# Performance work log

Hardware: AMD Instinct MI355X
Metric: run time of the kernel (lower is better)

Reference implementation:

```python
import jax, jax.numpy as jnp
import numpy as np

N = 4096
D = 512   # d_model == dff (required by the original code path)
H = 4
NEG = -1e10
ALPHA = 0.3  # keras LeakyReLU default alpha


def setup_inputs() -> dict:
    key = jax.random.key(0)
    ks = jax.random.split(key, 8)
    nodes = jax.random.normal(ks[0], (N, D), dtype=jnp.float32)
    # sparse-ish 0/1 dense adjacency with self loops
    adj = (jax.random.uniform(ks[1], (N, N)) < 0.01).astype(jnp.float32)
    adj = jnp.maximum(adj, jnp.eye(N, dtype=jnp.float32))
    s = 0.05
    W_node = jax.random.normal(ks[2], (D, D), dtype=jnp.float32) * s
    b_node = jnp.zeros((D,), dtype=jnp.float32)
    K = jax.random.normal(ks[3], (H, D, D), dtype=jnp.float32) * s
    A_self = jax.random.normal(ks[4], (H, D), dtype=jnp.float32) * s
    A_neigh = jax.random.normal(ks[5], (H, D), dtype=jnp.float32) * s
    return {"nodes": nodes, "adj": adj, "W_node": W_node, "b_node": b_node,
            "K": K, "A_self": A_self, "A_neigh": A_neigh, "num_heads": H}


def reference(nodes, adj, W_node, b_node, K, A_self, A_neigh, num_heads):
    # node_layer: Dense(dff)
    x = nodes @ W_node + b_node                       # [N, D]
    # per-head projection, vectorized over heads
    feats = jnp.einsum('nd,hdf->hnf', x, K)           # [H, N, D]
    # additive attention scores; both terms are per-row scalars -> [H, N]
    s = jnp.einsum('hnf,hf->hn', feats, A_self) + jnp.einsum('hnf,hf->hn', feats, A_neigh)
    s = jnp.where(s > 0, s, ALPHA * s)                # LeakyReLU(alpha=0.3)
    # broadcast row score over columns + adjacency mask, softmax over neighbors
    logits = s[:, :, None] + NEG * (1.0 - adj)[None]  # [H, N, N]
    attn = jax.nn.softmax(logits, axis=-1)
    # dropout is identity at inference (training=False)
    out = jnp.einsum('hij,hjf->hif', attn, feats)     # [H, N, D]
    out = jnp.mean(out, axis=0)                       # mean over heads
    return jax.nn.relu(out)
```

## Files before the change

kernel.cpp:

```cpp
#include <hip/hip_runtime.h>


typedef short  short8 __attribute__((ext_vector_type(8)));
typedef float  f32x4  __attribute__((ext_vector_type(4)));

__device__ inline unsigned short f2bf(float f) {
    union { float f; unsigned int u; } v; v.f = f;
    unsigned int u = v.u;
    u += 0x7fffu + ((u >> 16) & 1u);
    return (unsigned short)(u >> 16);
}

__device__ inline void gl_lds16(const void* gp, void* lp) {
    __builtin_amdgcn_global_load_lds(
        (const __attribute__((address_space(1))) void*)gp,
        (__attribute__((address_space(3))) void*)lp, 16, 0, 0);
}

__global__ __launch_bounds__(256) void prep_kernel(
        const float* __restrict__ nodes, const float* __restrict__ adj,
        const float* __restrict__ W, const float* __restrict__ b,
        const float* __restrict__ K,
        unsigned short* __restrict__ MmatT, float* __restrict__ bias2,
        unsigned short* __restrict__ nodesBf,
        int* __restrict__ degArr, int* __restrict__ nbrArr,
        int N, int D, int H, int numCast) {
    __shared__ unsigned short As[64][40];
    __shared__ unsigned short Bs[64][40];
    __shared__ float red[4][64];
    __shared__ int lst[1024];
    __shared__ int cnt;

    const int bid = blockIdx.x;
    const int tid = threadIdx.x;
    const int DD  = D * D;
    const int lane = tid & 63, wave = tid >> 6;
    const int wy = wave >> 1, wx = wave & 1;
    const int l15 = lane & 15, quad = lane >> 4;

    if (bid < 64) {
        const int by = bid >> 3, bx = bid & 7;
        const int f0 = by * 64, d0 = bx * 64;
        const float invH = 1.0f / (float)H;
        const int kk = tid >> 3;
        const int ff = (tid & 7) * 8;
        const int dr = tid >> 2;
        const int dk = (tid & 3) * 8;

        float4 kc[4][2], wc[2];
#pragma unroll
        for (int h = 0; h < 4; ++h) {
            const float* kp = K + ((size_t)h * D + kk) * D + f0 + ff;
            kc[h][0] = *reinterpret_cast<const float4*>(kp);
            kc[h][1] = *reinterpret_cast<const float4*>(kp + 4);
        }
        {
            const float* wp = W + (size_t)(d0 + dr) * D + dk;
            wc[0] = *reinterpret_cast<const float4*>(wp);
            wc[1] = *reinterpret_cast<const float4*>(wp + 4);
        }

        f32x4 acc[2][2] = {};
#pragma unroll
        for (int k0 = 0; k0 < 512; k0 += 32) {
            float4 kn[4][2], wn[2];
            if (k0 + 32 < 512) {
#pragma unroll
                for (int h = 0; h < 4; ++h) {
                    const float* kp = K + ((size_t)h * D + (k0 + 32 + kk)) * D + f0 + ff;
                    kn[h][0] = *reinterpret_cast<const float4*>(kp);
                    kn[h][1] = *reinterpret_cast<const float4*>(kp + 4);
                }
                const float* wp = W + (size_t)(d0 + dr) * D + (k0 + 32) + dk;
                wn[0] = *reinterpret_cast<const float4*>(wp);
                wn[1] = *reinterpret_cast<const float4*>(wp + 4);
            }
            float s[8];
#pragma unroll
            for (int j = 0; j < 4; ++j) {
                s[j]     = kc[0][0][j] + kc[1][0][j] + kc[2][0][j] + kc[3][0][j];
                s[j + 4] = kc[0][1][j] + kc[1][1][j] + kc[2][1][j] + kc[3][1][j];
            }
            short8 bv;
#pragma unroll
            for (int j = 0; j < 4; ++j) {
                bv[j]     = (short)f2bf(wc[0][j]);
                bv[j + 4] = (short)f2bf(wc[1][j]);
            }
            __syncthreads();
#pragma unroll
            for (int j = 0; j < 8; ++j)
                As[ff + j][kk] = f2bf(s[j] * invH);
            *reinterpret_cast<short8*>(&Bs[dr][dk]) = bv;
            __syncthreads();
            short8 a0 = *reinterpret_cast<const short8*>(&As[wy * 32 +      l15][quad * 8]);
            short8 a1 = *reinterpret_cast<const short8*>(&As[wy * 32 + 16 + l15][quad * 8]);
            short8 b0 = *reinterpret_cast<const short8*>(&Bs[wx * 32 +      l15][quad * 8]);
            short8 b1 = *reinterpret_cast<const short8*>(&Bs[wx * 32 + 16 + l15][quad * 8]);
            acc[0][0] = __builtin_amdgcn_mfma_f32_16x16x32_bf16(a0, b0, acc[0][0], 0, 0, 0);
            acc[0][1] = __builtin_amdgcn_mfma_f32_16x16x32_bf16(a0, b1, acc[0][1], 0, 0, 0);
            acc[1][0] = __builtin_amdgcn_mfma_f32_16x16x32_bf16(a1, b0, acc[1][0], 0, 0, 0);
            acc[1][1] = __builtin_amdgcn_mfma_f32_16x16x32_bf16(a1, b1, acc[1][1], 0, 0, 0);
            if (k0 + 32 < 512) {
#pragma unroll
                for (int h = 0; h < 4; ++h) { kc[h][0] = kn[h][0]; kc[h][1] = kn[h][1]; }
                wc[0] = wn[0]; wc[1] = wn[1];
            }
        }
#pragma unroll
        for (int mi = 0; mi < 2; ++mi)
#pragma unroll
            for (int ni = 0; ni < 2; ++ni) {
                int col = d0 + wx * 32 + ni * 16 + l15;
#pragma unroll
                for (int r = 0; r < 4; ++r) {
                    int row = f0 + wy * 32 + mi * 16 + quad * 4 + r;
                    MmatT[(size_t)row * D + col] = f2bf(acc[mi][ni][r]);
                }
            }
    } else if (bid < 72) {
        const int f0 = (bid - 64) * 64;
        const int fl = tid & 63, grp = tid >> 6;
        const float invH = 1.0f / (float)H;
        float a = 0.f;
        for (int d = grp; d < D; d += 4) {
            const float* kp = K + (size_t)d * D + f0 + fl;
            float v = 0.f;
#pragma unroll
            for (int h = 0; h < 4; ++h) v += kp[(size_t)h * DD];
            a += b[d] * v;
        }
        red[grp][fl] = a;
        __syncthreads();
        if (tid < 64)
            bias2[f0 + tid] = (red[0][tid] + red[1][tid] + red[2][tid] + red[3][tid]) * invH;
    } else if (bid < 72 + N) {
        const int row = bid - 72;
        if (tid == 0) cnt = 0;
        __syncthreads();
        const float4* ap = reinterpret_cast<const float4*>(adj + (size_t)row * N);
        float4 av[4];
#pragma unroll
        for (int c = 0; c < 4; ++c) av[c] = ap[c * 256 + tid];
#pragma unroll
        for (int c = 0; c < 4; ++c) {
            int b4 = (c * 256 + tid) * 4;
            if (av[c].x > 0.5f) { int p = atomicAdd(&cnt, 1); if (p < 1024) lst[p] = b4;     }
            if (av[c].y > 0.5f) { int p = atomicAdd(&cnt, 1); if (p < 1024) lst[p] = b4 + 1; }
            if (av[c].z > 0.5f) { int p = atomicAdd(&cnt, 1); if (p < 1024) lst[p] = b4 + 2; }
            if (av[c].w > 0.5f) { int p = atomicAdd(&cnt, 1); if (p < 1024) lst[p] = b4 + 3; }
        }
        __syncthreads();
        int deg = cnt; if (deg > 1024) deg = 1024;
        if (tid == 0) degArr[row] = deg;
        for (int i = tid; i < deg; i += 256)
            nbrArr[(size_t)row * 1024 + i] = lst[i];
    } else {
        const int total  = (N * D) >> 3;
        const int stride = numCast << 8;
        for (int i = (bid - 72 - N) * 256 + tid; i < total; i += stride) {
            const float* p = nodes + (size_t)i * 8;
            float4 x = *reinterpret_cast<const float4*>(p);
            float4 y = *reinterpret_cast<const float4*>(p + 4);
            short8 o;
            o[0] = (short)f2bf(x.x); o[1] = (short)f2bf(x.y);
            o[2] = (short)f2bf(x.z); o[3] = (short)f2bf(x.w);
            o[4] = (short)f2bf(y.x); o[5] = (short)f2bf(y.y);
            o[6] = (short)f2bf(y.z); o[7] = (short)f2bf(y.w);
            *reinterpret_cast<short8*>(nodesBf + (size_t)i * 8) = o;
        }
    }
}

__global__ __launch_bounds__(256) void gemm2_kernel(
        const unsigned short* __restrict__ nodesBf,
        const unsigned short* __restrict__ MmatT,
        const float* __restrict__ bias2, unsigned short* __restrict__ g, int D) {
    __shared__ unsigned short As[2][64][32];
    __shared__ unsigned short Bs[2][64][32];
    const int bid = blockIdx.x;
    const int lb = (bid & 7) * 64 + (bid >> 3);
    const int by = lb >> 3, bx = lb & 7;
    const int tid = threadIdx.x;
    const int lane = tid & 63, wave = tid >> 6;
    const int wy = wave >> 1, wx = wave & 1;
    const int l15 = lane & 15, quad = lane >> 4;

    const int cgl = ((tid & 3) ^ ((tid >> 3) & 3)) * 8;
    const unsigned short* Ag = nodesBf + (size_t)(by * 64 + (tid >> 2)) * D + cgl;
    const unsigned short* Bg = MmatT   + (size_t)(bx * 64 + (tid >> 2)) * D + cgl;
    unsigned short* AsW0 = &As[0][0][0] + wave * 512;
    unsigned short* AsW1 = &As[1][0][0] + wave * 512;
    unsigned short* BsW0 = &Bs[0][0][0] + wave * 512;
    unsigned short* BsW1 = &Bs[1][0][0] + wave * 512;

    f32x4 acc[2][2] = {};
    gl_lds16(Ag, AsW0);
    gl_lds16(Bg, BsW0);

    const int ra = wy * 32 + l15, rb = wx * 32 + l15;
    const int qa = (quad ^ ((ra >> 1) & 3)) * 8;
    const int qb = (quad ^ ((rb >> 1) & 3)) * 8;

    int cur = 0;
#pragma unroll
    for (int k0 = 0; k0 < 512; k0 += 32) {
        if (k0 + 32 < 512) {
            gl_lds16(Ag + k0 + 32, cur ? AsW0 : AsW1);
            gl_lds16(Bg + k0 + 32, cur ? BsW0 : BsW1);
            asm volatile("s_waitcnt vmcnt(2)" ::: "memory");
        } else {
            asm volatile("s_waitcnt vmcnt(0)" ::: "memory");
        }
        __builtin_amdgcn_s_barrier();
        __builtin_amdgcn_sched_barrier(0);
        const unsigned short* Af = cur ? &As[1][0][0] : &As[0][0][0];
        const unsigned short* Bf = cur ? &Bs[1][0][0] : &Bs[0][0][0];
        short8 a0 = *reinterpret_cast<const short8*>(Af + (ra     ) * 32 + qa);
        short8 a1 = *reinterpret_cast<const short8*>(Af + (ra + 16) * 32 + qa);
        short8 b0 = *reinterpret_cast<const short8*>(Bf + (rb     ) * 32 + qb);
        short8 b1 = *reinterpret_cast<const short8*>(Bf + (rb + 16) * 32 + qb);
        acc[0][0] = __builtin_amdgcn_mfma_f32_16x16x32_bf16(a0, b0, acc[0][0], 0, 0, 0);
        acc[0][1] = __builtin_amdgcn_mfma_f32_16x16x32_bf16(a0, b1, acc[0][1], 0, 0, 0);
        acc[1][0] = __builtin_amdgcn_mfma_f32_16x16x32_bf16(a1, b0, acc[1][0], 0, 0, 0);
        acc[1][1] = __builtin_amdgcn_mfma_f32_16x16x32_bf16(a1, b1, acc[1][1], 0, 0, 0);
        __builtin_amdgcn_sched_barrier(0);
        asm volatile("s_waitcnt lgkmcnt(0)" ::: "memory");
        __builtin_amdgcn_s_barrier();
        cur ^= 1;
    }

#pragma unroll
    for (int mi = 0; mi < 2; ++mi)
#pragma unroll
        for (int ni = 0; ni < 2; ++ni) {
            int col = bx * 64 + wx * 32 + ni * 16 + l15;
            float bvl = bias2[col];
#pragma unroll
            for (int r = 0; r < 4; ++r) {
                int row = by * 64 + wy * 32 + mi * 16 + quad * 4 + r;
                g[(size_t)row * D + col] = f2bf(acc[mi][ni][r] + bvl);
            }
        }
}

__global__ __launch_bounds__(256) void aggregate_kernel(
        const int* __restrict__ degArr, const int* __restrict__ nbrArr,
        const unsigned short* __restrict__ g, float* __restrict__ out,
        int N, int D) {
    const int row = blockIdx.x;
    const int tid = threadIdx.x;
    __shared__ int lst[1024];
    const int deg = degArr[row];
    for (int i = tid; i < deg; i += 256) lst[i] = nbrArr[(size_t)row * 1024 + i];
    __syncthreads();

    const int col = tid * 2;
    float acc0 = 0.f, acc1 = 0.f;
    int k = 0;
    for (; k + 8 <= deg; k += 8) {
        unsigned int u[8];
#pragma unroll
        for (int j = 0; j < 8; ++j)
            u[j] = *reinterpret_cast<const unsigned int*>(&g[(size_t)lst[k + j] * D + col]);
#pragma unroll
        for (int j = 0; j < 8; ++j) {
            union { unsigned int i; float f; } lo, hi;
            lo.i = u[j] << 16; hi.i = u[j] & 0xffff0000u;
            acc0 += lo.f; acc1 += hi.f;
        }
    }
    for (; k < deg; ++k) {
        unsigned int u = *reinterpret_cast<const unsigned int*>(&g[(size_t)lst[k] * D + col]);
        union { unsigned int i; float f; } lo, hi;
        lo.i = u << 16; hi.i = u & 0xffff0000u;
        acc0 += lo.f; acc1 += hi.f;
    }

    float inv = deg > 0 ? 1.f / (float)deg : 0.f;
    acc0 *= inv; acc1 *= inv;
    float2 o;
    o.x = acc0 > 0.f ? acc0 : 0.f;
    o.y = acc1 > 0.f ? acc1 : 0.f;
    *reinterpret_cast<float2*>(&out[(size_t)row * D + col]) = o;
}

extern "C" void kernel_launch(void* const* d_in, const int* in_sizes, int n_in,
                              void* d_out, int out_size, void* d_ws, size_t ws_size,
                              hipStream_t stream) {
    const float* nodes  = (const float*)d_in[0];
    const float* adj    = (const float*)d_in[1];
    const float* W_node = (const float*)d_in[2];
    const float* b_node = (const float*)d_in[3];
    const float* K      = (const float*)d_in[4];

    const int D  = in_sizes[3];
    const int N  = in_sizes[0] / D;
    const int H  = in_sizes[4] / (D * D);
    const int DD = D * D;

    float* out = (float*)d_out;

    char* ws = (char*)d_ws;
    unsigned short* MmatT   = (unsigned short*)(ws);
    size_t off = (size_t)DD * 2;
    float*          bias2   = (float*)(ws + off);          off += (size_t)D * 4;
    unsigned short* nodesBf = (unsigned short*)(ws + off); off += (size_t)N * D * 2;
    unsigned short* g_bf16  = (unsigned short*)(ws + off); off += (size_t)N * D * 2;
    int*            degArr  = (int*)(ws + off);            off += (size_t)N * 4;
    int*            nbrArr  = (int*)(ws + off);

    const int numCast = 952;
    prep_kernel<<<dim3(64 + 8 + N + numCast), 256, 0, stream>>>(
        nodes, adj, W_node, b_node, K, MmatT, bias2, nodesBf, degArr, nbrArr,
        N, D, H, numCast);

    gemm2_kernel<<<dim3((N / 64) * (D / 64)), 256, 0, stream>>>(
        nodesBf, MmatT, bias2, g_bf16, D);

    aggregate_kernel<<<dim3(N), 256, 0, stream>>>(degArr, nbrArr, g_bf16, out, N, D);
}
```

Measured before the change: 158.6 us.

## Double prep kernel block size and split weight-fold GEMM K across two halves

Launches the prep kernel with 512 threads per block. In the weight-fold GEMM, the two 256-thread halves each handle half of the K dimension, and the partial tiles are combined through shared memory. The adjacency scan and cast blocks now read 8 floats per thread, and the bias reduction uses 8 groups. The cast grid shrinks to 512 blocks. The GEMM loses its register prefetch and adds a reduction step, and the shared-memory union changes occupancy.

```diff
diff --git a/kernel.cpp b/kernel.cpp
--- a/kernel.cpp
+++ b/kernel.cpp
@@ -17,7 +17,7 @@
         (__attribute__((address_space(3))) void*)lp, 16, 0, 0);
 }
 
-__global__ __launch_bounds__(256) void prep_kernel(
+__global__ __launch_bounds__(512, 4) void prep_kernel(
         const float* __restrict__ nodes, const float* __restrict__ adj,
         const float* __restrict__ W, const float* __restrict__ b,
         const float* __restrict__ K,
@@ -25,148 +25,163 @@
         unsigned short* __restrict__ nodesBf,
         int* __restrict__ degArr, int* __restrict__ nbrArr,
         int N, int D, int H, int numCast) {
-    __shared__ unsigned short As[64][40];
-    __shared__ unsigned short Bs[64][40];
-    __shared__ float red[4][64];
-    __shared__ int lst[1024];
+    __shared__ union {
+        struct {
+            unsigned short As[2][64][40];
+            unsigned short Bs[2][64][40];
+        } g;
+        float red64[64][64];
+        int   lst[1024];
+    } sm;
+    __shared__ float red2[8][64];
     __shared__ int cnt;
 
     const int bid = blockIdx.x;
     const int tid = threadIdx.x;
     const int DD  = D * D;
     const int lane = tid & 63, wave = tid >> 6;
-    const int wy = wave >> 1, wx = wave & 1;
     const int l15 = lane & 15, quad = lane >> 4;
 
     if (bid < 64) {
         const int by = bid >> 3, bx = bid & 7;
         const int f0 = by * 64, d0 = bx * 64;
         const float invH = 1.0f / (float)H;
-        const int kk = tid >> 3;
-        const int ff = (tid & 7) * 8;
-        const int dr = tid >> 2;
-        const int dk = (tid & 3) * 8;
-
-        float4 kc[4][2], wc[2];
-#pragma unroll
-        for (int h = 0; h < 4; ++h) {
-            const float* kp = K + ((size_t)h * D + kk) * D + f0 + ff;
-            kc[h][0] = *reinterpret_cast<const float4*>(kp);
-            kc[h][1] = *reinterpret_cast<const float4*>(kp + 4);
-        }
-        {
-            const float* wp = W + (size_t)(d0 + dr) * D + dk;
-            wc[0] = *reinterpret_cast<const float4*>(wp);
-            wc[1] = *reinterpret_cast<const float4*>(wp + 4);
-        }
+        const int h  = tid >> 8;
+        const int th = tid & 255;
+        const int wy = (wave >> 1) & 1, wx = wave & 1;
+        const int kk = th >> 3;
+        const int ff = (th & 7) * 8;
+        const int dr = th >> 2;
+        const int dk = (th & 3) * 8;
+        const int kh = h * 256;
 
         f32x4 acc[2][2] = {};
-#pragma unroll
-        for (int k0 = 0; k0 < 512; k0 += 32) {
-            float4 kn[4][2], wn[2];
-            if (k0 + 32 < 512) {
-#pragma unroll
-                for (int h = 0; h < 4; ++h) {
-                    const float* kp = K + ((size_t)h * D + (k0 + 32 + kk)) * D + f0 + ff;
-                    kn[h][0] = *reinterpret_cast<const float4*>(kp);
-                    kn[h][1] = *reinterpret_cast<const float4*>(kp + 4);
-                }
-                const float* wp = W + (size_t)(d0 + dr) * D + (k0 + 32) + dk;
-                wn[0] = *reinterpret_cast<const float4*>(wp);
-                wn[1] = *reinterpret_cast<const float4*>(wp + 4);
-            }
+        for (int k0 = 0; k0 < 256; k0 += 32) {
+            f32x4 kv[4][2];
+#pragma unroll
+            for (int hh = 0; hh < 4; ++hh) {
+                const float* kp = K + ((size_t)hh * D + (kh + k0 + kk)) * D + f0 + ff;
+                kv[hh][0] = *reinterpret_cast<const f32x4*>(kp);
+                kv[hh][1] = *reinterpret_cast<const f32x4*>(kp + 4);
+            }
+            const float* wp = W + (size_t)(d0 + dr) * D + kh + k0 + dk;
+            f32x4 wu = *reinterpret_cast<const f32x4*>(wp);
+            f32x4 wv = *reinterpret_cast<const f32x4*>(wp + 4);
+
             float s[8];
 #pragma unroll
             for (int j = 0; j < 4; ++j) {
-                s[j]     = kc[0][0][j] + kc[1][0][j] + kc[2][0][j] + kc[3][0][j];
-                s[j + 4] = kc[0][1][j] + kc[1][1][j] + kc[2][1][j] + kc[3][1][j];
+                s[j]     = kv[0][0][j] + kv[1][0][j] + kv[2][0][j] + kv[3][0][j];
+                s[j + 4] = kv[0][1][j] + kv[1][1][j] + kv[2][1][j] + kv[3][1][j];
             }
             short8 bv;
 #pragma unroll
             for (int j = 0; j < 4; ++j) {
-                bv[j]     = (short)f2bf(wc[0][j]);
-                bv[j + 4] = (short)f2bf(wc[1][j]);
+                bv[j]     = (short)f2bf(wu[j]);
+                bv[j + 4] = (short)f2bf(wv[j]);
             }
             __syncthreads();
 #pragma unroll
             for (int j = 0; j < 8; ++j)
-                As[ff + j][kk] = f2bf(s[j] * invH);
-            *reinterpret_cast<short8*>(&Bs[dr][dk]) = bv;
+                sm.g.As[h][ff + j][kk] = f2bf(s[j] * invH);
+            *reinterpret_cast<short8*>(&sm.g.Bs[h][dr][dk]) = bv;
             __syncthreads();
-            short8 a0 = *reinterpret_cast<const short8*>(&As[wy * 32 +      l15][quad * 8]);
-            short8 a1 = *reinterpret_cast<const short8*>(&As[wy * 32 + 16 + l15][quad * 8]);
-            short8 b0 = *reinterpret_cast<const short8*>(&Bs[wx * 32 +      l15][quad * 8]);
-            short8 b1 = *reinterpret_cast<const short8*>(&Bs[wx * 32 + 16 + l15][quad * 8]);
+            short8 a0 = *reinterpret_cast<const short8*>(&sm.g.As[h][wy * 32 +      l15][quad * 8]);
+            short8 a1 = *reinterpret_cast<const short8*>(&sm.g.As[h][wy * 32 + 16 + l15][quad * 8]);
+            short8 b0 = *reinterpret_cast<const short8*>(&sm.g.Bs[h][wx * 32 +      l15][quad * 8]);
+            short8 b1 = *reinterpret_cast<const short8*>(&sm.g.Bs[h][wx * 32 + 16 + l15][quad * 8]);
             acc[0][0] = __builtin_amdgcn_mfma_f32_16x16x32_bf16(a0, b0, acc[0][0], 0, 0, 0);
             acc[0][1] = __builtin_amdgcn_mfma_f32_16x16x32_bf16(a0, b1, acc[0][1], 0, 0, 0);
             acc[1][0] = __builtin_amdgcn_mfma_f32_16x16x32_bf16(a1, b0, acc[1][0], 0, 0, 0);
             acc[1][1] = __builtin_amdgcn_mfma_f32_16x16x32_bf16(a1, b1, acc[1][1], 0, 0, 0);
-            if (k0 + 32 < 512) {
-#pragma unroll
-                for (int h = 0; h < 4; ++h) { kc[h][0] = kn[h][0]; kc[h][1] = kn[h][1]; }
-                wc[0] = wn[0]; wc[1] = wn[1];
-            }
-        }
-#pragma unroll
-        for (int mi = 0; mi < 2; ++mi)
-#pragma unroll
-            for (int ni = 0; ni < 2; ++ni) {
-                int col = d0 + wx * 32 + ni * 16 + l15;
-#pragma unroll
-                for (int r = 0; r < 4; ++r) {
-                    int row = f0 + wy * 32 + mi * 16 + quad * 4 + r;
-                    MmatT[(size_t)row * D + col] = f2bf(acc[mi][ni][r]);
+        }
+        __syncthreads();
+        if (h == 1) {
+#pragma unroll
+            for (int mi = 0; mi < 2; ++mi)
+#pragma unroll
+                for (int ni = 0; ni < 2; ++ni)
+#pragma unroll
+                    for (int r = 0; r < 4; ++r)
+                        sm.red64[wy * 32 + mi * 16 + quad * 4 + r]
+                                [wx * 32 + ni * 16 + l15] = acc[mi][ni][r];
+        }
+        __syncthreads();
+        if (h == 0) {
+#pragma unroll
+            for (int mi = 0; mi < 2; ++mi)
+#pragma unroll
+                for (int ni = 0; ni < 2; ++ni) {
+                    int col = d0 + wx * 32 + ni * 16 + l15;
+#pragma unroll
+                    for (int r = 0; r < 4; ++r) {
+                        int row = f0 + wy * 32 + mi * 16 + quad * 4 + r;
+                        float v = acc[mi][ni][r] +
+                            sm.red64[wy * 32 + mi * 16 + quad * 4 + r]
+                                    [wx * 32 + ni * 16 + l15];
+                        MmatT[(size_t)row * D + col] = f2bf(v);
+                    }
                 }
-            }
+        }
     } else if (bid < 72) {
         const int f0 = (bid - 64) * 64;
         const int fl = tid & 63, grp = tid >> 6;
         const float invH = 1.0f / (float)H;
         float a = 0.f;
-        for (int d = grp; d < D; d += 4) {
-            const float* kp = K + (size_t)d * D + f0 + fl;
-            float v = 0.f;
-#pragma unroll
-            for (int h = 0; h < 4; ++h) v += kp[(size_t)h * DD];
-            a += b[d] * v;
-        }
-        red[grp][fl] = a;
-        __syncthreads();
-        if (tid < 64)
-            bias2[f0 + tid] = (red[0][tid] + red[1][tid] + red[2][tid] + red[3][tid]) * invH;
+        for (int d0i = grp * 64; d0i < grp * 64 + 64; d0i += 4) {
+            float v[4] = {0.f, 0.f, 0.f, 0.f};
+#pragma unroll
+            for (int dd = 0; dd < 4; ++dd)
+#pragma unroll
+                for (int hh = 0; hh < 4; ++hh)
+                    v[dd] += K[((size_t)hh * D + d0i + dd) * D + f0 + fl];
+#pragma unroll
+            for (int dd = 0; dd < 4; ++dd) a += b[d0i + dd] * v[dd];
+        }
+        red2[grp][fl] = a;
+        __syncthreads();
+        if (tid < 64) {
+            float s = 0.f;
+#pragma unroll
+            for (int gg = 0; gg < 8; ++gg) s += red2[gg][tid];
+            bias2[f0 + tid] = s * invH;
+        }
     } else if (bid < 72 + N) {
         const int row = bid - 72;
         if (tid == 0) cnt = 0;
         __syncthreads();
-        const float4* ap = reinterpret_cast<const float4*>(adj + (size_t)row * N);
-        float4 av[4];
-#pragma unroll
-        for (int c = 0; c < 4; ++c) av[c] = ap[c * 256 + tid];
-#pragma unroll
-        for (int c = 0; c < 4; ++c) {
-            int b4 = (c * 256 + tid) * 4;
-            if (av[c].x > 0.5f) { int p = atomicAdd(&cnt, 1); if (p < 1024) lst[p] = b4;     }
-            if (av[c].y > 0.5f) { int p = atomicAdd(&cnt, 1); if (p < 1024) lst[p] = b4 + 1; }
-            if (av[c].z > 0.5f) { int p = atomicAdd(&cnt, 1); if (p < 1024) lst[p] = b4 + 2; }
-            if (av[c].w > 0.5f) { int p = atomicAdd(&cnt, 1); if (p < 1024) lst[p] = b4 + 3; }
+        const f32x4* ap = reinterpret_cast<const f32x4*>(adj + (size_t)row * N + tid * 8);
+        f32x4 av[2];
+        av[0] = ap[0];
+        av[1] = ap[1];
+#pragma unroll
+        for (int c = 0; c < 2; ++c) {
+            int b4 = tid * 8 + c * 4;
+#pragma unroll
+            for (int j = 0; j < 4; ++j)
+                if (av[c][j] > 0.5f) {
+                    int p = atomicAdd(&cnt, 1);
+                    if (p < 1024) sm.lst[p] = b4 + j;
+                }
         }
         __syncthreads();
         int deg = cnt; if (deg > 1024) deg = 1024;
         if (tid == 0) degArr[row] = deg;
-        for (int i = tid; i < deg; i += 256)
-            nbrArr[(size_t)row * 1024 + i] = lst[i];
+        for (int i = tid; i < deg; i += 512)
+            nbrArr[(size_t)row * 1024 + i] = sm.lst[i];
     } else {
         const int total  = (N * D) >> 3;
-        const int stride = numCast << 8;
-        for (int i = (bid - 72 - N) * 256 + tid; i < total; i += stride) {
+        const int stride = numCast << 9;
+        for (int i = (bid - 72 - N) * 512 + tid; i < total; i += stride) {
             const float* p = nodes + (size_t)i * 8;
-            float4 x = *reinterpret_cast<const float4*>(p);
-            float4 y = *reinterpret_cast<const float4*>(p + 4);
+            f32x4 x = *reinterpret_cast<const f32x4*>(p);
+            f32x4 y = *reinterpret_cast<const f32x4*>(p + 4);
             short8 o;
-            o[0] = (short)f2bf(x.x); o[1] = (short)f2bf(x.y);
-            o[2] = (short)f2bf(x.z); o[3] = (short)f2bf(x.w);
-            o[4] = (short)f2bf(y.x); o[5] = (short)f2bf(y.y);
-            o[6] = (short)f2bf(y.z); o[7] = (short)f2bf(y.w);
+#pragma unroll
+            for (int j = 0; j < 4; ++j) {
+                o[j]     = (short)f2bf(x[j]);
+                o[j + 4] = (short)f2bf(y[j]);
+            }
             *reinterpret_cast<short8*>(nodesBf + (size_t)i * 8) = o;
         }
     }
@@ -310,8 +325,8 @@
     int*            degArr  = (int*)(ws + off);            off += (size_t)N * 4;
     int*            nbrArr  = (int*)(ws + off);
 
-    const int numCast = 952;
-    prep_kernel<<<dim3(64 + 8 + N + numCast), 256, 0, stream>>>(
+    const int numCast = 512;
+    prep_kernel<<<dim3(64 + 8 + N + numCast), 512, 0, stream>>>(
         nodes, adj, W_node, b_node, K, MmatT, bias2, nodesBf, degArr, nbrArr,
         N, D, H, numCast);
 
```

New measurement: 148.7 us. 1.07x faster.
